# Optimization experiments

Hardware: AMD Instinct MI355X
Metric: run time of the kernel (lower is better)

## Reference

```python
import jax, jax.numpy as jnp
import numpy as np

B, T, D, H = 64, 257, 1024, 16
F = 4096
R = 16
HD = D // H


def _layer_norm(x, g, b, eps=1e-5):
    mu = x.mean(-1, keepdims=True)
    var = x.var(-1, keepdims=True)
    return (x - mu) / jnp.sqrt(var + eps) * g + b


def _quick_gelu(x):
    return x * jax.nn.sigmoid(1.702 * x)


def _attention(x, Wq, bq, Wk, bk, Wv, bv, Wo, bo):
    scale = HD ** -0.5
    q = (x @ Wq + bq) * scale
    k = x @ Wk + bk
    v = x @ Wv + bv
    q = q.reshape(B, T, H, HD).transpose(0, 2, 1, 3)
    k = k.reshape(B, T, H, HD).transpose(0, 2, 1, 3)
    v = v.reshape(B, T, H, HD).transpose(0, 2, 1, 3)
    attn = jax.nn.softmax(jnp.einsum('bhqd,bhkd->bhqk', q, k), axis=-1)
    o = jnp.einsum('bhqk,bhkd->bhqd', attn, v)
    o = o.transpose(0, 2, 1, 3).reshape(B, T, D)
    return o @ Wo + bo


def _match_indices(metric, r, class_token=True):
    # cosine-normalized bipartite matching (no-grad path in torch; index-only here)
    m = metric / jnp.linalg.norm(metric, axis=-1, keepdims=True)
    a, b = m[:, ::2, :], m[:, 1::2, :]        # [B, ta, D], [B, tb, D]
    scores = jnp.einsum('nac,nbc->nab', a, b)  # [B, ta, tb]
    if class_token:
        scores = scores.at[:, 0, :].set(-jnp.inf)
    node_max = scores.max(-1)
    node_idx = scores.argmax(-1)
    edge_idx = jnp.argsort(-node_max, axis=-1)  # descending
    unm_idx = edge_idx[:, r:]
    src_idx = edge_idx[:, :r]
    dst_idx = jnp.take_along_axis(node_idx, src_idx, axis=-1)
    if class_token:
        unm_idx = jnp.sort(unm_idx, axis=1)
    return unm_idx, src_idx, dst_idx


def _merge_sum(x, unm_idx, src_idx, dst_idx):
    src, dst = x[:, ::2, :], x[:, 1::2, :]
    c = x.shape[-1]
    unm = jnp.take_along_axis(src, unm_idx[..., None], axis=1)       # [B, ta-r, c]
    sel = jnp.take_along_axis(src, src_idx[..., None], axis=1)       # [B, r, c]
    dst = jax.vmap(lambda d, di, sv: d.at[di].add(sv))(dst, dst_idx, sel)
    return jnp.concatenate([unm, dst], axis=1)                       # [B, T-r, c]


def setup_inputs() -> dict:
    key = jax.random.key(0)
    ks = jax.random.split(key, 12)
    s = 0.02
    return {
        'hidden_states': jax.random.normal(ks[0], (B, T, D), jnp.float32),
        'ln1_g': jnp.ones((D,), jnp.float32),
        'ln1_b': jnp.zeros((D,), jnp.float32),
        'Wq': jax.random.normal(ks[1], (D, D), jnp.float32) * s,
        'bq': jnp.zeros((D,), jnp.float32),
        'Wk': jax.random.normal(ks[2], (D, D), jnp.float32) * s,
        'bk': jnp.zeros((D,), jnp.float32),
        'Wv': jax.random.normal(ks[3], (D, D), jnp.float32) * s,
        'bv': jnp.zeros((D,), jnp.float32),
        'Wo': jax.random.normal(ks[4], (D, D), jnp.float32) * s,
        'bo': jnp.zeros((D,), jnp.float32),
        'ln2_g': jnp.ones((D,), jnp.float32),
        'ln2_b': jnp.zeros((D,), jnp.float32),
        'W1': jax.random.normal(ks[5], (D, F), jnp.float32) * s,
        'b1': jnp.zeros((F,), jnp.float32),
        'W2': jax.random.normal(ks[6], (F, D), jnp.float32) * s,
        'b2': jnp.zeros((D,), jnp.float32),
    }


def reference(hidden_states, ln1_g, ln1_b, Wq, bq, Wk, bk, Wv, bv, Wo, bo,
              ln2_g, ln2_b, W1, b1, W2, b2):
    # 1) LN1 + self-attention + residual
    x = hidden_states + _attention(_layer_norm(hidden_states, ln1_g, ln1_b),
                                   Wq, bq, Wk, bk, Wv, bv, Wo, bo)
    # 2) ToMe merge with weighted average (initial size = ones -> merge_wavg)
    metric = jax.lax.stop_gradient(x)
    unm_idx, src_idx, dst_idx = _match_indices(metric, R, class_token=True)
    size = jnp.ones((B, T, 1), x.dtype)
    x = _merge_sum(x * size, unm_idx, src_idx, dst_idx)
    size = _merge_sum(size, unm_idx, src_idx, dst_idx)
    x = x / size
    # 3) LN2 + MLP (quick_gelu) + residual
    h = _layer_norm(x, ln2_g, ln2_b)
    h = _quick_gelu(h @ W1 + b1) @ W2 + b2
    return x + h  # [B, T - R, D]
```

## Files before the change

kernel.cpp:

```cpp
#include <hip/hip_runtime.h>
#include <math.h>

#define BB 64
#define TT 257
#define DD 1024
#define HH 16
#define FF 4096
#define RR 16
#define HDD 64
#define TMM 241
#define M1 (BB*TT)
#define M2 (BB*TMM)
#define NA 129
#define NB 128

typedef float f4v __attribute__((ext_vector_type(4)));
typedef short s8v __attribute__((ext_vector_type(8)));
typedef short s4v __attribute__((ext_vector_type(4)));
typedef unsigned short us;

__device__ __forceinline__ us f2bf(float f){
  unsigned u = __float_as_uint(f);
  u += 0x7fffu + ((u >> 16) & 1u);
  return (us)(u >> 16);
}
__device__ __forceinline__ float bf2f(us h){
  return __uint_as_float(((unsigned)h) << 16);
}
__device__ __forceinline__ void splitpk(float f0, float f1, unsigned &hp, unsigned &lp){
  unsigned u0 = __float_as_uint(f0), u1 = __float_as_uint(f1);
  unsigned h0m = u0 & 0xFFFF0000u, h1m = u1 & 0xFFFF0000u;
  hp = (u0 >> 16) | h1m;
  float l0 = f0 - __uint_as_float(h0m);
  float l1 = f1 - __uint_as_float(h1m);
  lp = (__float_as_uint(l0) >> 16) | (__float_as_uint(l1) & 0xFFFF0000u);
}
__device__ __forceinline__ void gl16(const us* g, us* l){
  __builtin_amdgcn_global_load_lds((const __attribute__((address_space(1))) void*)g,
                                   (__attribute__((address_space(3))) void*)l, 16, 0, 0);
}

__global__ __launch_bounds__(64) void lnstats_kernel(const float* __restrict__ x,
                                                     float* __restrict__ st)
{
  int row = blockIdx.x, lane = threadIdx.x;
  const float* p = x + (size_t)row * DD;
  float s = 0.0f, sq = 0.0f;
  #pragma unroll
  for (int i = 0; i < 4; i++){
    float4 v = *(const float4*)(p + i * 256 + lane * 4);
    s  += v.x + v.y + v.z + v.w;
    sq += v.x*v.x + v.y*v.y + v.z*v.z + v.w*v.w;
  }
  #pragma unroll
  for (int m = 1; m < 64; m <<= 1){ s += __shfl_xor(s, m); sq += __shfl_xor(sq, m); }
  if (lane == 0){
    float mu  = s * (1.0f / DD);
    float var = sq * (1.0f / DD) - mu * mu;
    st[2*row]     = mu;
    st[2*row + 1] = 1.0f / sqrtf(var + 1e-5f);
  }
}

__global__ __launch_bounds__(256) void lncvt_kernel(const float* __restrict__ x,
    const float* __restrict__ st, const float* __restrict__ g,
    const float* __restrict__ b, us* __restrict__ out)
{
  int row = blockIdx.x, tid = threadIdx.x;
  float mu = st[2*row], rstd = st[2*row + 1];
  float4 xv = *(const float4*)(x + (size_t)row * DD + tid * 4);
  float4 gv = *(const float4*)(g + tid * 4);
  float4 bv = *(const float4*)(b + tid * 4);
  s4v o;
  o[0] = (short)f2bf((xv.x - mu) * rstd * gv.x + bv.x);
  o[1] = (short)f2bf((xv.y - mu) * rstd * gv.y + bv.y);
  o[2] = (short)f2bf((xv.z - mu) * rstd * gv.z + bv.z);
  o[3] = (short)f2bf((xv.w - mu) * rstd * gv.w + bv.w);
  *(s4v*)(out + (size_t)row * DD + tid * 4) = o;
}

__global__ __launch_bounds__(256) void wt_kernel(const float* __restrict__ src,
                                                 us* __restrict__ dhi,
                                                 us* __restrict__ dlo,
                                                 const float* __restrict__ gscale,
                                                 int K, int N)
{
  __shared__ float t[32][33];
  int tx = threadIdx.x, ty = threadIdx.y;
  int n0 = blockIdx.x * 32, k0 = blockIdx.y * 32;
  #pragma unroll
  for (int r = 0; r < 4; r++)
    t[ty + 8*r][tx] = src[(size_t)(k0 + ty + 8*r) * N + n0 + tx];
  __syncthreads();
  float gs = gscale ? gscale[k0 + tx] : 1.0f;
  #pragma unroll
  for (int r = 0; r < 4; r++){
    float f = t[tx][ty + 8*r] * gs;
    us hi = f2bf(f);
    size_t o = (size_t)(n0 + ty + 8*r) * K + k0 + tx;
    dhi[o] = hi;
    if (dlo) dlo[o] = f2bf(f - bf2f(hi));
  }
}

__global__ __launch_bounds__(256) void qc_kernel(const float* __restrict__ Wq,
    const float* __restrict__ Wk, const float* __restrict__ Wv,
    const float* __restrict__ g, const float* __restrict__ b,
    float* __restrict__ c1, float* __restrict__ c2)
{
  __shared__ float p1[4][64], p2[4][64];
  int n0 = blockIdx.x * 64;
  int kind = n0 >> 10, col0 = n0 & 1023;
  const float* W = (kind == 0) ? Wq : (kind == 1) ? Wk : Wv;
  int tx = threadIdx.x & 63, ty = threadIdx.x >> 6;
  float s1 = 0.0f, s2 = 0.0f;
  for (int k = ty; k < 1024; k += 4){
    float w = W[(size_t)k * 1024 + col0 + tx];
    s1 += g[k] * w;
    s2 += b[k] * w;
  }
  p1[ty][tx] = s1; p2[ty][tx] = s2;
  __syncthreads();
  if (ty == 0){
    c1[n0 + tx] = p1[0][tx] + p1[1][tx] + p1[2][tx] + p1[3][tx];
    c2[n0 + tx] = p2[0][tx] + p2[1][tx] + p2[2][tx] + p2[3][tx];
  }
}

__global__ __launch_bounds__(512) void qkv_kernel(const float* __restrict__ hidden,
    const us* __restrict__ WBh, const us* __restrict__ WBl,
    const float* __restrict__ bq, const float* __restrict__ bk, const float* __restrict__ bv,
    const float* __restrict__ lnstat, const float* __restrict__ c1, const float* __restrict__ c2,
    us* __restrict__ qhp, us* __restrict__ qlp, us* __restrict__ khp,
    us* __restrict__ klp, us* __restrict__ vhp, us* __restrict__ vlp)
{
  const int M = M1, K = DD;
  __shared__ __align__(16) us Ah[128*40];
  __shared__ __align__(16) us Al[128*40];
  __shared__ __align__(16) us Bh[256*32];
  __shared__ __align__(16) us Bl[256*32];
  int tid = threadIdx.x;
  int m0 = blockIdx.y * 128, n0 = blockIdx.x * 256;
  int lane = tid & 63, w = tid >> 6;
  int wr = w >> 2, wc = w & 3;
  int fr = lane & 15, fq = lane >> 4;
  f4v acc[4][4];
  f4v zero = {0.0f, 0.0f, 0.0f, 0.0f};
  #pragma unroll
  for (int i = 0; i < 4; i++)
    #pragma unroll
    for (int j = 0; j < 4; j++) acc[i][j] = zero;
  int sr = tid >> 2, sc4 = (tid & 3) * 8;
  int ar = m0 + sr; if (ar >= M) ar = M - 1;
  int lr = lane >> 2, lc = (lane & 3) * 8;
  int gb0 = n0 + w*32 + lr;
  int swl = ((lr >> 1) & 3) << 3;
  int swr = ((fr >> 1) & 3) << 3;

  for (int kk = 0; kk < K; kk += 32){
    {
      const float* ap = hidden + (size_t)ar * K + kk + sc4;
      float4 fa = *(const float4*)(ap);
      float4 fb = *(const float4*)(ap + 4);
      unsigned h0, h1, h2, h3, l0, l1, l2, l3;
      splitpk(fa.x, fa.y, h0, l0);
      splitpk(fa.z, fa.w, h1, l1);
      splitpk(fb.x, fb.y, h2, l2);
      splitpk(fb.z, fb.w, h3, l3);
      uint4 hv = {h0, h1, h2, h3};
      uint4 lv = {l0, l1, l2, l3};
      *(uint4*)&Ah[sr*40 + sc4] = hv;
      *(uint4*)&Al[sr*40 + sc4] = lv;
    }
    gl16(WBh + (size_t)gb0 * K + kk + (lc ^ swl),        &Bh[(w*32)*32]);
    gl16(WBh + (size_t)(gb0 + 16) * K + kk + (lc ^ swl), &Bh[(w*32 + 16)*32]);
    gl16(WBl + (size_t)gb0 * K + kk + (lc ^ swl),        &Bl[(w*32)*32]);
    gl16(WBl + (size_t)(gb0 + 16) * K + kk + (lc ^ swl), &Bl[(w*32 + 16)*32]);
    __syncthreads();
    s8v ah[4], bh[4], al[4], bl[4];
    #pragma unroll
    for (int m = 0; m < 4; m++){
      ah[m] = *(const s8v*)&Ah[(wr*64 + m*16 + fr)*40 + fq*8];
      al[m] = *(const s8v*)&Al[(wr*64 + m*16 + fr)*40 + fq*8];
    }
    #pragma unroll
    for (int n = 0; n < 4; n++){
      bh[n] = *(const s8v*)&Bh[(wc*64 + n*16 + fr)*32 + (fq*8 ^ swr)];
      bl[n] = *(const s8v*)&Bl[(wc*64 + n*16 + fr)*32 + (fq*8 ^ swr)];
    }
    #pragma unroll
    for (int m = 0; m < 4; m++)
      #pragma unroll
      for (int n = 0; n < 4; n++){
        acc[m][n] = __builtin_amdgcn_mfma_f32_16x16x32_bf16(ah[m], bh[n], acc[m][n], 0, 0, 0);
        acc[m][n] = __builtin_amdgcn_mfma_f32_16x16x32_bf16(ah[m], bl[n], acc[m][n], 0, 0, 0);
        acc[m][n] = __builtin_amdgcn_mfma_f32_16x16x32_bf16(al[m], bh[n], acc[m][n], 0, 0, 0);
      }
    __syncthreads();
  }
  int kind = n0 >> 10;
  const float* bsel = (kind == 0) ? bq : (kind == 1) ? bk : bv;
  us* O0 = (kind == 0) ? qhp : (kind == 1) ? khp : vhp;
  us* O1 = (kind == 0) ? qlp : (kind == 1) ? klp : vlp;
  float scl = (kind == 0) ? 0.125f : 1.0f;
  float C1r[4], C2r[4];
  int h2r[4], d2r[4];
  #pragma unroll
  for (int n = 0; n < 4; n++){
    int gcol = n0 + wc*64 + n*16 + fr;
    int lcn = gcol & 1023;
    h2r[n] = lcn >> 6; d2r[n] = lcn & 63;
    C1r[n] = c1[gcol];
    C2r[n] = c2[gcol] + bsel[lcn];
  }
  #pragma unroll
  for (int m = 0; m < 4; m++){
    int grow0 = m0 + wr*64 + m*16 + fq*4;
    #pragma unroll
    for (int i = 0; i < 4; i++){
      int grow = grow0 + i;
      if (grow < M){
        float mu = lnstat[2*grow], rstd = lnstat[2*grow + 1];
        int b2 = grow / 257, t2 = grow - b2 * 257;
        size_t rb = ((size_t)(b2*16) * 257 + t2) * 64;
        #pragma unroll
        for (int n = 0; n < 4; n++){
          size_t off2 = rb + (size_t)h2r[n] * (257*64) + d2r[n];
          float v = (rstd * acc[m][n][i] - rstd * mu * C1r[n] + C2r[n]) * scl;
          us hi = f2bf(v);
          O0[off2] = hi;
          O1[off2] = f2bf(v - bf2f(hi));
        }
      }
    }
  }
}

template<int AMODE, int SPLIT, int EPI>
__global__ __launch_bounds__(256) void gemm2_kernel(const us* __restrict__ Ahp,
    const us* __restrict__ Alp,
    const us* __restrict__ BTh, const us* __restrict__ BTl,
    const float* __restrict__ bias, const float* __restrict__ resid,
    void* __restrict__ C0, int M, int N, int K)
{
  __shared__ __align__(16) us Ah[128*32];
  __shared__ __align__(16) us Bh[128*32];
  __shared__ __align__(16) us Al[SPLIT ? 128*32 : 8];
  __shared__ __align__(16) us Bl[SPLIT ? 128*32 : 8];
  int tid = threadIdx.x;
  int m0 = blockIdx.y * 128, n0 = blockIdx.x * 128;
  int lane = tid & 63, w = tid >> 6;
  int wr = w >> 1, wc = w & 1;
  int fr = lane & 15, fq = lane >> 4;
  f4v acc[4][4];
  f4v zero = {0.0f, 0.0f, 0.0f, 0.0f};
  #pragma unroll
  for (int i = 0; i < 4; i++)
    #pragma unroll
    for (int j = 0; j < 4; j++) acc[i][j] = zero;
  int lr = lane >> 2, lc = (lane & 3) * 8;
  int swl = ((lr >> 1) & 3) << 3;
  int swr = ((fr >> 1) & 3) << 3;
  int ga0 = m0 + w*32 + lr;      if (ga0 >= M) ga0 = M - 1;
  int ga1 = m0 + w*32 + 16 + lr; if (ga1 >= M) ga1 = M - 1;
  int gb0 = n0 + w*32 + lr;
  int b2a = ga0 / 257, t2a = ga0 - b2a * 257;
  int b2b = ga1 / 257, t2b = ga1 - b2b * 257;

  for (int kk = 0; kk < K; kk += 32){
    if (AMODE == 1){
      gl16(Ahp + (size_t)ga0 * K + kk + (lc ^ swl), &Ah[(w*32)*32]);
      gl16(Ahp + (size_t)ga1 * K + kk + (lc ^ swl), &Ah[(w*32 + 16)*32]);
      if (SPLIT){
        gl16(Alp + (size_t)ga0 * K + kk + (lc ^ swl), &Al[(w*32)*32]);
        gl16(Alp + (size_t)ga1 * K + kk + (lc ^ swl), &Al[(w*32 + 16)*32]);
      }
    } else {
      int h2 = kk >> 6, d2 = (kk & 63) + (lc ^ swl);
      size_t o0 = ((size_t)(b2a*16 + h2) * 257 + t2a) * 64 + d2;
      size_t o1 = ((size_t)(b2b*16 + h2) * 257 + t2b) * 64 + d2;
      gl16(Ahp + o0, &Ah[(w*32)*32]);
      gl16(Ahp + o1, &Ah[(w*32 + 16)*32]);
      if (SPLIT){
        gl16(Alp + o0, &Al[(w*32)*32]);
        gl16(Alp + o1, &Al[(w*32 + 16)*32]);
      }
    }
    gl16(BTh + (size_t)gb0 * K + kk + (lc ^ swl),        &Bh[(w*32)*32]);
    gl16(BTh + (size_t)(gb0 + 16) * K + kk + (lc ^ swl), &Bh[(w*32 + 16)*32]);
    if (SPLIT){
      gl16(BTl + (size_t)gb0 * K + kk + (lc ^ swl),        &Bl[(w*32)*32]);
      gl16(BTl + (size_t)(gb0 + 16) * K + kk + (lc ^ swl), &Bl[(w*32 + 16)*32]);
    }
    __syncthreads();
    s8v ah[4], bh[4], al[4], bl[4];
    #pragma unroll
    for (int m = 0; m < 4; m++){
      ah[m] = *(const s8v*)&Ah[(wr*64 + m*16 + fr)*32 + (fq*8 ^ swr)];
      if (SPLIT) al[m] = *(const s8v*)&Al[(wr*64 + m*16 + fr)*32 + (fq*8 ^ swr)];
    }
    #pragma unroll
    for (int n = 0; n < 4; n++){
      bh[n] = *(const s8v*)&Bh[(wc*64 + n*16 + fr)*32 + (fq*8 ^ swr)];
      if (SPLIT) bl[n] = *(const s8v*)&Bl[(wc*64 + n*16 + fr)*32 + (fq*8 ^ swr)];
    }
    #pragma unroll
    for (int m = 0; m < 4; m++)
      #pragma unroll
      for (int n = 0; n < 4; n++){
        acc[m][n] = __builtin_amdgcn_mfma_f32_16x16x32_bf16(ah[m], bh[n], acc[m][n], 0, 0, 0);
        if (SPLIT){
          acc[m][n] = __builtin_amdgcn_mfma_f32_16x16x32_bf16(ah[m], bl[n], acc[m][n], 0, 0, 0);
          acc[m][n] = __builtin_amdgcn_mfma_f32_16x16x32_bf16(al[m], bh[n], acc[m][n], 0, 0, 0);
        }
      }
    __syncthreads();
  }
  #pragma unroll
  for (int m = 0; m < 4; m++){
    int grow0 = m0 + wr*64 + m*16 + fq*4;
    #pragma unroll
    for (int n = 0; n < 4; n++){
      int gcol = n0 + wc*64 + n*16 + fr;
      float bcol = bias[gcol];
      #pragma unroll
      for (int i = 0; i < 4; i++){
        int grow = grow0 + i;
        if (grow < M){
          float v = acc[m][n][i] + bcol;
          size_t off = (size_t)grow * N + gcol;
          if (EPI == 1){
            ((float*)C0)[off] = v + resid[off];
          } else {
            float gq = v / (1.0f + expf(-1.702f * v));
            ((us*)C0)[off] = f2bf(gq);
          }
        }
      }
    }
  }
}

template<int EPI>
__global__ __launch_bounds__(512) void gemm8p_kernel(const us* __restrict__ A,
    const us* __restrict__ B, const float* __restrict__ bias,
    const float* __restrict__ resid, void* __restrict__ C, int M, int N, int K)
{
  __shared__ __align__(16) us As[3][256*32];
  __shared__ __align__(16) us Bs[3][256*32];
  int tid = threadIdx.x;
  int m0 = blockIdx.y * 256, n0 = blockIdx.x * 256;
  int lane = tid & 63, w = tid >> 6;
  int wr = w >> 2, wc = w & 3;
  int fr = lane & 15, fq = lane >> 4;
  f4v acc[8][4];
  f4v zero = {0.0f, 0.0f, 0.0f, 0.0f};
  #pragma unroll
  for (int i = 0; i < 8; i++)
    #pragma unroll
    for (int j = 0; j < 4; j++) acc[i][j] = zero;
  int srow = w*16 + (lane >> 2);
  int aR0 = m0 + srow;        if (aR0 >= M) aR0 = M - 1;
  int aR1 = m0 + 128 + srow;  if (aR1 >= M) aR1 = M - 1;
  int bR0 = n0 + srow;
  int bR1 = n0 + 128 + srow;
  int o16 = ((lane & 3) * 8) ^ (((srow >> 1) & 3) << 3);
  int swr = ((fr >> 1) & 3) << 3;
  int ldst = w * 512;

  const int NT = K >> 5;
  #pragma unroll
  for (int t0 = 0; t0 < 2; t0++){
    gl16(A + (size_t)aR0 * K + t0*32 + o16, &As[t0][ldst]);
    gl16(B + (size_t)bR0 * K + t0*32 + o16, &Bs[t0][ldst]);
    gl16(A + (size_t)aR1 * K + t0*32 + o16, &As[t0][4096 + ldst]);
    gl16(B + (size_t)bR1 * K + t0*32 + o16, &Bs[t0][4096 + ldst]);
  }
  asm volatile("s_waitcnt vmcnt(4)" ::: "memory");
  __builtin_amdgcn_s_barrier();

  int buf = 0;
  #pragma unroll 1
  for (int t = 0; t < NT; ++t){
    int nbuf = buf + 2; if (nbuf >= 3) nbuf -= 3;
    bool pf = (t + 2) < NT;
    int kk2 = (t + 2) * 32;
    us* Ab = As[buf];
    us* Bb = Bs[buf];
    {
      s8v a[4], b[4];
      #pragma unroll
      for (int mt = 0; mt < 4; mt++){
        int r = wr*128 + mt*16 + fr;
        a[mt] = *(const s8v*)&Ab[r*32 + (fq*8 ^ swr)];
      }
      #pragma unroll
      for (int nt = 0; nt < 4; nt++){
        int r = wc*64 + nt*16 + fr;
        b[nt] = *(const s8v*)&Bb[r*32 + (fq*8 ^ swr)];
      }
      if (pf){
        gl16(A + (size_t)aR0 * K + kk2 + o16, &As[nbuf][ldst]);
        gl16(B + (size_t)bR0 * K + kk2 + o16, &Bs[nbuf][ldst]);
      }
      __builtin_amdgcn_s_barrier();
      __builtin_amdgcn_s_setprio(1);
      #pragma unroll
      for (int mt = 0; mt < 4; mt++)
        #pragma unroll
        for (int nt = 0; nt < 4; nt++)
          acc[mt][nt] = __builtin_amdgcn_mfma_f32_16x16x32_bf16(a[mt], b[nt], acc[mt][nt], 0, 0, 0);
      __builtin_amdgcn_s_setprio(0);
      __builtin_amdgcn_s_barrier();
    }
    {
      s8v a[4], b[4];
      #pragma unroll
      for (int mt = 0; mt < 4; mt++){
        int r = wr*128 + 64 + mt*16 + fr;
        a[mt] = *(const s8v*)&Ab[r*32 + (fq*8 ^ swr)];
      }
      #pragma unroll
      for (int nt = 0; nt < 4; nt++){
        int r = wc*64 + nt*16 + fr;
        b[nt] = *(const s8v*)&Bb[r*32 + (fq*8 ^ swr)];
      }
      if (pf){
        gl16(A + (size_t)aR1 * K + kk2 + o16, &As[nbuf][4096 + ldst]);
        gl16(B + (size_t)bR1 * K + kk2 + o16, &Bs[nbuf][4096 + ldst]);
      }
      __builtin_amdgcn_s_barrier();
      __builtin_amdgcn_s_setprio(1);
      #pragma unroll
      for (int mt = 0; mt < 4; mt++)
        #pragma unroll
        for (int nt = 0; nt < 4; nt++)
          acc[4 + mt][nt] = __builtin_amdgcn_mfma_f32_16x16x32_bf16(a[mt], b[nt], acc[4 + mt][nt], 0, 0, 0);
      __builtin_amdgcn_s_setprio(0);
    }
    if (t + 1 < NT){
      if (pf) asm volatile("s_waitcnt vmcnt(4)" ::: "memory");
      else    asm volatile("s_waitcnt vmcnt(0)" ::: "memory");
    }
    __builtin_amdgcn_s_barrier();
    buf = buf + 1; if (buf >= 3) buf = 0;
  }
  #pragma unroll
  for (int mh = 0; mh < 2; mh++)
    #pragma unroll
    for (int mt = 0; mt < 4; mt++){
      int grow0 = m0 + wr*128 + mh*64 + mt*16 + fq*4;
      #pragma unroll
      for (int nt = 0; nt < 4; nt++){
        int gcol = n0 + wc*64 + nt*16 + fr;
        float bcol = bias[gcol];
        #pragma unroll
        for (int i = 0; i < 4; i++){
          int grow = grow0 + i;
          if (grow < M){
            float v = acc[mh*4 + mt][nt][i] + bcol;
            size_t off = (size_t)grow * N + gcol;
            if (EPI == 1){
              ((float*)C)[off] = v + resid[off];
            } else {
              float gq = v / (1.0f + expf(-1.702f * v));
              ((us*)C)[off] = f2bf(gq);
            }
          }
        }
      }
    }
}

__global__ __launch_bounds__(512, 1) void attn_flash_kernel(
    const us* __restrict__ Qh, const us* __restrict__ Ql,
    const us* __restrict__ Kh, const us* __restrict__ Klo,
    const us* __restrict__ Vh, const us* __restrict__ Vlo,
    us* Oh, us* Ol)
{
  __shared__ __align__(16) us Kl[257 * 128];
  __shared__ __align__(16) us Vl[64 * 640];
  int bh = blockIdx.x;
  const size_t hb = (size_t)bh * 257 * 64;
  int tid = threadIdx.x;
  int l = tid & 63, w = tid >> 6;
  int g = l >> 4, c = l & 15;
  const float NEG = -3.0e38f;

  {
    s8v z8 = {0,0,0,0,0,0,0,0};
    for (int idx = tid; idx < 64*640/8; idx += 512)
      *((s8v*)Vl + idx) = z8;
  }
  __syncthreads();
  for (int idx = tid; idx < 257*8; idx += 512){
    int tok = idx >> 3, ch = idx & 7;
    int sw = (tok & 7) << 4;
    s8v hv = *(const s8v*)(Kh  + hb + (size_t)tok * 64 + ch*8);
    s8v lv = *(const s8v*)(Klo + hb + (size_t)tok * 64 + ch*8);
    char* kr = (char*)Kl + tok * 256;
    *(s8v*)(kr + ((ch*16) ^ sw)) = hv;
    *(s8v*)(kr + 128 + ((ch*16) ^ sw)) = lv;
  }
  for (int idx = tid; idx < 257*8; idx += 512){
    int tok = idx >> 3, ch = idx & 7;
    s8v hv = *(const s8v*)(Vh  + hb + (size_t)tok * 64 + ch*8);
    s8v lv = *(const s8v*)(Vlo + hb + (size_t)tok * 64 + ch*8);
    #pragma unroll
    for (int j = 0; j < 8; j++){
      int d = ch*8 + j;
      char* vr = (char*)Vl + d * 1280;
      int off = (tok * 2) ^ (j << 4);
      *(us*)(vr + off) = (us)hv[j];
      *(us*)(vr + 640 + off) = (us)lv[j];
    }
  }
  __syncthreads();

  for (int qt = w; qt < 17; qt += 8){
    int t0 = qt * 16;
    int qr = t0 + c; if (qr > 256) qr = 256;
    const us* qp  = Qh + hb + (size_t)qr * 64 + g*8;
    const us* qp2 = Ql + hb + (size_t)qr * 64 + g*8;
    s8v qhi[2], qlo[2];
    qhi[0] = *(const s8v*)(qp);       qhi[1] = *(const s8v*)(qp + 32);
    qlo[0] = *(const s8v*)(qp2);      qlo[1] = *(const s8v*)(qp2 + 32);

    float m_run = NEG, l_run = 0.0f;
    f4v o4[4];
    #pragma unroll
    for (int dt = 0; dt < 4; dt++) o4[dt] = (f4v){0.0f, 0.0f, 0.0f, 0.0f};

    #pragma unroll 1
    for (int mck = 0; mck < 9; mck++){
      f4v a0, a1;
      {
        int t = 2*mck;
        int krow = t * 16 + c; if (krow > 256) krow = 256;
        char* kr = (char*)Kl + krow * 256;
        int sw = (krow & 7) << 4;
        s8v khi0 = *(const s8v*)(kr + ((g * 16) ^ sw));
        s8v khi1 = *(const s8v*)(kr + ((64 + g * 16) ^ sw));
        s8v klo0 = *(const s8v*)(kr + 128 + ((g * 16) ^ sw));
        s8v klo1 = *(const s8v*)(kr + 128 + ((64 + g * 16) ^ sw));
        f4v a = {0.0f, 0.0f, 0.0f, 0.0f};
        a = __builtin_amdgcn_mfma_f32_16x16x32_bf16(khi0, qhi[0], a, 0, 0, 0);
        a = __builtin_amdgcn_mfma_f32_16x16x32_bf16(khi1, qhi[1], a, 0, 0, 0);
        a = __builtin_amdgcn_mfma_f32_16x16x32_bf16(khi0, qlo[0], a, 0, 0, 0);
        a = __builtin_amdgcn_mfma_f32_16x16x32_bf16(khi1, qlo[1], a, 0, 0, 0);
        a = __builtin_amdgcn_mfma_f32_16x16x32_bf16(klo0, qhi[0], a, 0, 0, 0);
        a = __builtin_amdgcn_mfma_f32_16x16x32_bf16(klo1, qhi[1], a, 0, 0, 0);
        a0 = a;
      }
      if (mck < 8){
        int t = 2*mck + 1;
        int krow = t * 16 + c; if (krow > 256) krow = 256;
        char* kr = (char*)Kl + krow * 256;
        int sw = (krow & 7) << 4;
        s8v khi0 = *(const s8v*)(kr + ((g * 16) ^ sw));
        s8v khi1 = *(const s8v*)(kr + ((64 + g * 16) ^ sw));
        s8v klo0 = *(const s8v*)(kr + 128 + ((g * 16) ^ sw));
        s8v klo1 = *(const s8v*)(kr + 128 + ((64 + g * 16) ^ sw));
        f4v a = {0.0f, 0.0f, 0.0f, 0.0f};
        a = __builtin_amdgcn_mfma_f32_16x16x32_bf16(khi0, qhi[0], a, 0, 0, 0);
        a = __builtin_amdgcn_mfma_f32_16x16x32_bf16(khi1, qhi[1], a, 0, 0, 0);
        a = __builtin_amdgcn_mfma_f32_16x16x32_bf16(khi0, qlo[0], a, 0, 0, 0);
        a = __builtin_amdgcn_mfma_f32_16x16x32_bf16(khi1, qlo[1], a, 0, 0, 0);
        a = __builtin_amdgcn_mfma_f32_16x16x32_bf16(klo0, qhi[0], a, 0, 0, 0);
        a = __builtin_amdgcn_mfma_f32_16x16x32_bf16(klo1, qhi[1], a, 0, 0, 0);
        a1 = a;
      } else {
        a1 = (f4v){NEG, NEG, NEG, NEG};
        a0[0] = (g == 0) ? a0[0] : NEG;
        a0[1] = NEG; a0[2] = NEG; a0[3] = NEG;
      }
      float cm = fmaxf(fmaxf(fmaxf(a0[0], a0[1]), fmaxf(a0[2], a0[3])),
                       fmaxf(fmaxf(a1[0], a1[1]), fmaxf(a1[2], a1[3])));
      cm = fmaxf(cm, __shfl_xor(cm, 16));
      cm = fmaxf(cm, __shfl_xor(cm, 32));
      float m_new = fmaxf(m_run, cm);
      float scl = __expf(m_run - m_new);
      m_run = m_new;
      l_run *= scl;
      #pragma unroll
      for (int dt = 0; dt < 4; dt++){
        o4[dt][0] *= scl; o4[dt][1] *= scl; o4[dt][2] *= scl; o4[dt][3] *= scl;
      }
      float ls = 0.0f;
      unsigned Ph2[2][2], Pl2[2][2];
      #pragma unroll
      for (int k2 = 0; k2 < 2; k2++){
        float e0 = __expf(a0[2*k2] - m_new), e1 = __expf(a0[2*k2+1] - m_new);
        ls += e0 + e1;
        us h0 = f2bf(e0), h1 = f2bf(e1);
        Ph2[0][k2] = (unsigned)h0 | ((unsigned)h1 << 16);
        Pl2[0][k2] = (unsigned)f2bf(e0 - bf2f(h0)) | ((unsigned)f2bf(e1 - bf2f(h1)) << 16);
        float e2 = __expf(a1[2*k2] - m_new), e3 = __expf(a1[2*k2+1] - m_new);
        ls += e2 + e3;
        us h2 = f2bf(e2), h3 = f2bf(e3);
        Ph2[1][k2] = (unsigned)h2 | ((unsigned)h3 << 16);
        Pl2[1][k2] = (unsigned)f2bf(e2 - bf2f(h2)) | ((unsigned)f2bf(e3 - bf2f(h3)) << 16);
      }
      l_run += ls;
      s8v pbh, pbl;
      #pragma unroll
      for (int ww = 0; ww < 4; ww++){
        int srcl = (((g & 1) * 2 + (ww >> 1)) << 4) | c;
        unsigned h0 = (unsigned)__shfl((int)Ph2[0][ww & 1], srcl, 64);
        unsigned lo0 = (unsigned)__shfl((int)Pl2[0][ww & 1], srcl, 64);
        unsigned h1 = (unsigned)__shfl((int)Ph2[1][ww & 1], srcl, 64);
        unsigned lo1 = (unsigned)__shfl((int)Pl2[1][ww & 1], srcl, 64);
        ((unsigned*)&pbh)[ww] = (g >> 1) ? h1 : h0;
        ((unsigned*)&pbl)[ww] = (g >> 1) ? lo1 : lo0;
      }
      #pragma unroll
      for (int dt = 0; dt < 4; dt++){
        int d = dt * 16 + c;
        char* vr = (char*)Vl + d * 1280;
        int off = (mck * 64 + g * 16) ^ ((d & 7) << 4);
        s8v vh = *(const s8v*)(vr + off);
        s8v vlo = *(const s8v*)(vr + 640 + off);
        o4[dt] = __builtin_amdgcn_mfma_f32_16x16x32_bf16(vh, pbh, o4[dt], 0, 0, 0);
        o4[dt] = __builtin_amdgcn_mfma_f32_16x16x32_bf16(vh, pbl, o4[dt], 0, 0, 0);
        o4[dt] = __builtin_amdgcn_mfma_f32_16x16x32_bf16(vlo, pbh, o4[dt], 0, 0, 0);
      }
    }
    l_run += __shfl_xor(l_run, 16);
    l_run += __shfl_xor(l_run, 32);
    float inv = 1.0f / l_run;
    int qrow = t0 + c;
    if (qrow <= 256){
      us* oph = Oh + hb + (size_t)qrow * 64;
      us* opl = Ol + hb + (size_t)qrow * 64;
      #pragma unroll
      for (int dt = 0; dt < 4; dt++){
        s4v hv4, lv4;
        #pragma unroll
        for (int i = 0; i < 4; i++){
          float ov = o4[dt][i] * inv;
          us hi = f2bf(ov);
          hv4[i] = (short)hi;
          lv4[i] = (short)f2bf(ov - bf2f(hi));
        }
        *(s4v*)(oph + dt*16 + g*4) = hv4;
        *(s4v*)(opl + dt*16 + g*4) = lv4;
      }
    }
  }
}

__global__ __launch_bounds__(64) void norms_kernel(const float* __restrict__ x, float* __restrict__ nrm)
{
  int row = blockIdx.x, lane = threadIdx.x;
  const float* p = x + (size_t)row * DD;
  float sq = 0.0f;
  #pragma unroll
  for (int i = 0; i < 4; i++){
    float4 v = *(const float4*)(p + i * 256 + lane * 4);
    sq += v.x*v.x + v.y*v.y + v.z*v.z + v.w*v.w;
  }
  #pragma unroll
  for (int m = 1; m < 64; m <<= 1) sq += __shfl_xor(sq, m);
  if (lane == 0) nrm[row] = sqrtf(sq);
}

__global__ __launch_bounds__(256) void scores_kernel(const float* __restrict__ x,
                                                     const float* __restrict__ nrm,
                                                     float* __restrict__ sc)
{
  __shared__ __align__(16) float as_[16][1028];
  __shared__ __align__(16) float bs_[16][1028];
  int it = blockIdx.x, b = blockIdx.y;
  int tid = threadIdx.x;
  int rloc = tid >> 4, chunk = tid & 15;
  {
    int i = it * 16 + rloc;
    int tg = (i < NA) ? 2 * i : 2 * (NA - 1);
    const float* p = x + ((size_t)b * TT + tg) * DD + chunk * 64;
    #pragma unroll
    for (int ii = 0; ii < 16; ii++)
      *(float4*)&as_[rloc][chunk * 64 + 4*ii] = *(const float4*)(p + 4*ii);
  }
  for (int jt = 0; jt < 8; jt++){
    __syncthreads();
    {
      int j = jt * 16 + rloc;
      const float* p = x + ((size_t)b * TT + 2*j + 1) * DD + chunk * 64;
      #pragma unroll
      for (int ii = 0; ii < 16; ii++)
        *(float4*)&bs_[rloc][chunk * 64 + 4*ii] = *(const float4*)(p + 4*ii);
    }
    __syncthreads();
    int iloc = tid >> 4, jloc = tid & 15;
    float sum = 0.0f;
    #pragma unroll 8
    for (int cgg = 0; cgg < 1024; cgg += 4){
      float4 av = *(const float4*)&as_[iloc][cgg];
      float4 bvv = *(const float4*)&bs_[jloc][cgg];
      sum += av.x*bvv.x + av.y*bvv.y + av.z*bvv.z + av.w*bvv.w;
    }
    int i = it * 16 + iloc, j = jt * 16 + jloc;
    if (i < NA){
      float val = sum / (nrm[(size_t)b * TT + 2*i] * nrm[(size_t)b * TT + 2*j + 1]);
      sc[((size_t)b * NA + i) * NB + j] = val;
    }
  }
}

__global__ __launch_bounds__(64) void node_kernel(const float* __restrict__ sc,
                                                  float* __restrict__ nmax, int* __restrict__ nidx)
{
  int i = blockIdx.x, b = blockIdx.y, lane = threadIdx.x;
  const float* row = sc + ((size_t)b * NA + i) * NB;
  float v0 = row[lane];
  float v1 = row[lane + 64];
  float bv = v0; int bi = lane;
  if (v1 > bv){ bv = v1; bi = lane + 64; }
  #pragma unroll
  for (int m = 1; m < 64; m <<= 1){
    float ov = __shfl_xor(bv, m);
    int oi = __shfl_xor(bi, m);
    if (ov > bv || (ov == bv && oi < bi)){ bv = ov; bi = oi; }
  }
  if (lane == 0){
    if (i == 0){ nmax[(size_t)b * NA] = -INFINITY; nidx[(size_t)b * NA] = 0; }
    else { nmax[(size_t)b * NA + i] = bv; nidx[(size_t)b * NA + i] = bi; }
  }
}

__global__ __launch_bounds__(256) void rank_kernel(const float* __restrict__ nmax,
    const int* __restrict__ nidx, int* __restrict__ src, int* __restrict__ dst,
    int* __restrict__ unm, int* __restrict__ cnt)
{
  __shared__ float v[NA];
  __shared__ int rk[NA];
  __shared__ int edge[NA];
  __shared__ int cs[NB];
  int b = blockIdx.x, t = threadIdx.x;
  if (t < NA) v[t] = nmax[(size_t)b * NA + t];
  if (t < NB) cs[t] = 0;
  __syncthreads();
  if (t < NA){
    float vt = v[t]; int r = 0;
    for (int i = 0; i < NA; i++){
      float vi = v[i];
      r += (vi > vt) || (vi == vt && i < t);
    }
    rk[t] = r; edge[r] = t;
  }
  __syncthreads();
  if (t < RR){
    int s = edge[t];
    src[b * RR + t] = s;
    int d = nidx[(size_t)b * NA + s];
    dst[b * RR + t] = d;
    atomicAdd(&cs[d], 1);
  }
  if (t < NA && rk[t] >= RR){
    int p = 0;
    for (int i = 0; i < NA; i++) p += (i < t) && (rk[i] >= RR);
    unm[b * (NA - RR) + p] = t;
  }
  __syncthreads();
  if (t < NB) cnt[b * NB + t] = cs[t];
}

__global__ __launch_bounds__(256) void merge_kernel(const float* __restrict__ x,
    const int* __restrict__ src, const int* __restrict__ dst, const int* __restrict__ unm,
    const int* __restrict__ cnt, float* __restrict__ xm)
{
  int u = blockIdx.x, b = blockIdx.y;
  int c = threadIdx.x * 4;
  const float* xb = x + (size_t)b * TT * DD;
  float4 acc;
  if (u < NA - RR){
    int ts = 2 * unm[b * (NA - RR) + u];
    acc = *(const float4*)(xb + (size_t)ts * DD + c);
  } else {
    int j = u - (NA - RR);
    acc = *(const float4*)(xb + (size_t)(2*j + 1) * DD + c);
    #pragma unroll
    for (int k2 = 0; k2 < RR; k2++){
      if (dst[b * RR + k2] == j){
        int ts = 2 * src[b * RR + k2];
        float4 av = *(const float4*)(xb + (size_t)ts * DD + c);
        acc.x += av.x; acc.y += av.y; acc.z += av.z; acc.w += av.w;
      }
    }
    float inv = 1.0f / (float)(1 + cnt[b * NB + j]);
    acc.x *= inv; acc.y *= inv; acc.z *= inv; acc.w *= inv;
  }
  *(float4*)(xm + ((size_t)b * TMM + u) * DD + c) = acc;
}

extern "C" void kernel_launch(void* const* d_in, const int* in_sizes, int n_in,
                              void* d_out, int out_size, void* d_ws, size_t ws_size,
                              hipStream_t stream)
{
  (void)in_sizes; (void)n_in; (void)out_size; (void)ws_size;
  const float* hidden = (const float*)d_in[0];
  const float* ln1_g  = (const float*)d_in[1];
  const float* ln1_b  = (const float*)d_in[2];
  const float* Wq = (const float*)d_in[3];
  const float* bq = (const float*)d_in[4];
  const float* Wk = (const float*)d_in[5];
  const float* bk = (const float*)d_in[6];
  const float* Wv = (const float*)d_in[7];
  const float* bv = (const float*)d_in[8];
  const float* Wo = (const float*)d_in[9];
  const float* bo = (const float*)d_in[10];
  const float* ln2_g = (const float*)d_in[11];
  const float* ln2_b = (const float*)d_in[12];
  const float* W1 = (const float*)d_in[13];
  const float* b1 = (const float*)d_in[14];
  const float* W2 = (const float*)d_in[15];
  const float* b2 = (const float*)d_in[16];

  char* base = (char*)d_ws;
  const size_t PE = (size_t)M1 * DD;
  const size_t PL = PE * sizeof(us);
  us* qh = (us*)base;          us* ql = qh + PE;
  us* kh = (us*)(base + 2*PL); us* kl = kh + PE;
  us* vh = (us*)(base + 4*PL); us* vl = vh + PE;
  us* wts = (us*)(base + 6*PL);
  const size_t WD = (size_t)DD * DD;
  us* wqh = wts;
  us* wkh = wqh + WD;
  us* wvh = wkh + WD;
  us* wql = wvh + WD;
  us* wkl = wql + WD;
  us* wvl = wkl + WD;
  us* woh = wvl + WD;
  us* wol = woh + WD;
  us* w1h = wol + WD;
  us* w2h = w1h + (size_t)DD * FF;
  float* lnst1 = (float*)(w2h + (size_t)FF * DD);
  float* c1p   = lnst1 + 2 * M1;
  float* c2p   = c1p + 3072;
  float* xb = (float*)(base + 2*PL);
  float* nrm   = (float*)(base + 4*PL);
  float* sc    = nrm + M1;
  float* nmaxp = sc + (size_t)BB * NA * NB;
  int*   nidxp = (int*)(nmaxp + BB * NA);
  int*   srcI  = nidxp + BB * NA;
  int*   dstI  = srcI + BB * RR;
  int*   unmI  = dstI + BB * RR;
  int*   cntI  = unmI + BB * (NA - RR);
  us*    xh2   = (us*)(base + 4*PL + (size_t)8*1024*1024);
  float* lnst2 = (float*)(base + 4*PL + (size_t)48*1024*1024);
  float* xm = (float*)d_out;
  us* mid = (us*)base;

  dim3 tb32(32, 8);
  wt_kernel<<<dim3(DD/32, DD/32), tb32, 0, stream>>>(Wq, wqh, wql, ln1_g, DD, DD);
  wt_kernel<<<dim3(DD/32, DD/32), tb32, 0, stream>>>(Wk, wkh, wkl, ln1_g, DD, DD);
  wt_kernel<<<dim3(DD/32, DD/32), tb32, 0, stream>>>(Wv, wvh, wvl, ln1_g, DD, DD);
  wt_kernel<<<dim3(DD/32, DD/32), tb32, 0, stream>>>(Wo, woh, wol, nullptr, DD, DD);
  wt_kernel<<<dim3(FF/32, DD/32), tb32, 0, stream>>>(W1, w1h, nullptr, nullptr, DD, FF);
  wt_kernel<<<dim3(DD/32, FF/32), tb32, 0, stream>>>(W2, w2h, nullptr, nullptr, FF, DD);

  qc_kernel<<<48, 256, 0, stream>>>(Wq, Wk, Wv, ln1_g, ln1_b, c1p, c2p);
  lnstats_kernel<<<M1, 64, 0, stream>>>(hidden, lnst1);

  qkv_kernel<<<dim3(3072/256, (M1 + 127)/128), 512, 0, stream>>>(hidden, wqh, wql,
      bq, bk, bv, lnst1, c1p, c2p, qh, ql, kh, kl, vh, vl);

  attn_flash_kernel<<<BB*HH, 512, 0, stream>>>(qh, ql, kh, kl, vh, vl, qh, ql);

  gemm2_kernel<2,1,1><<<dim3(DD/128, (M1 + 127)/128), 256, 0, stream>>>(qh, ql, woh, wol,
      bo, hidden, xb, M1, DD, DD);

  norms_kernel<<<M1, 64, 0, stream>>>(xb, nrm);
  scores_kernel<<<dim3(9, BB), 256, 0, stream>>>(xb, nrm, sc);
  node_kernel<<<dim3(NA, BB), 64, 0, stream>>>(sc, nmaxp, nidxp);
  rank_kernel<<<BB, 256, 0, stream>>>(nmaxp, nidxp, srcI, dstI, unmI, cntI);
  merge_kernel<<<dim3(TMM, BB), 256, 0, stream>>>(xb, srcI, dstI, unmI, cntI, xm);

  lnstats_kernel<<<M2, 64, 0, stream>>>(xm, lnst2);
  lncvt_kernel<<<M2, 256, 0, stream>>>(xm, lnst2, ln2_g, ln2_b, xh2);

  gemm8p_kernel<2><<<dim3(FF/256, (M2 + 255)/256), 512, 0, stream>>>(xh2, w1h,
      b1, nullptr, mid, M2, FF, DD);
  gemm8p_kernel<1><<<dim3(DD/256, (M2 + 255)/256), 512, 0, stream>>>(mid, w2h,
      b2, xm, (float*)d_out, M2, DD, FF);
}
```

Before: 1.559 ms.

## Compute ToMe similarity scores with split-bf16 MFMA instead of fp32 FMA

The output projection epilogue now stores the residual-added activations as a hi/lo bf16 pair instead of fp32. The cosine-similarity scores are then computed by a new MFMA kernel that uses three bf16 products (hh, hl, lh) to approximate fp32 accuracy, replacing the scalar fp32 dot-product kernel. The norms and merge kernels read the split pair and reconstruct fp32. The change moves the scores work onto matrix cores and halves per-tensor byte width, at the cost of two extra MFMAs per tile, a small loss of precision in the reconstructed activations, and only 128 blocks for the scores launch.

After: 1.392 ms, median of 2. 1.12x faster.

```diff
diff --git a/kernel.cpp b/kernel.cpp
--- a/kernel.cpp
+++ b/kernel.cpp
@@ -34,6 +34,12 @@
   float l0 = f0 - __uint_as_float(h0m);
   float l1 = f1 - __uint_as_float(h1m);
   lp = (__float_as_uint(l0) >> 16) | (__float_as_uint(l1) & 0xFFFF0000u);
+}
+__device__ __forceinline__ void split1(float f, us &h, us &l){
+  unsigned u = __float_as_uint(f);
+  unsigned hm = u & 0xFFFF0000u;
+  h = (us)(u >> 16);
+  l = (us)(__float_as_uint(f - __uint_as_float(hm)) >> 16);
 }
 __device__ __forceinline__ void gl16(const us* g, us* l){
   __builtin_amdgcn_global_load_lds((const __attribute__((address_space(1))) void*)g,
@@ -241,7 +247,7 @@
     const us* __restrict__ Alp,
     const us* __restrict__ BTh, const us* __restrict__ BTl,
     const float* __restrict__ bias, const float* __restrict__ resid,
-    void* __restrict__ C0, int M, int N, int K)
+    void* __restrict__ C0, void* __restrict__ C1, int M, int N, int K)
 {
   __shared__ __align__(16) us Ah[128*32];
   __shared__ __align__(16) us Bh[128*32];
@@ -331,9 +337,15 @@
           size_t off = (size_t)grow * N + gcol;
           if (EPI == 1){
             ((float*)C0)[off] = v + resid[off];
-          } else {
+          } else if (EPI == 2){
             float gq = v / (1.0f + expf(-1.702f * v));
             ((us*)C0)[off] = f2bf(gq);
+          } else {
+            float x = v + resid[off];
+            us h, l;
+            split1(x, h, l);
+            ((us*)C0)[off] = h;
+            ((us*)C1)[off] = l;
           }
         }
       }
@@ -649,60 +661,103 @@
   }
 }
 
-__global__ __launch_bounds__(64) void norms_kernel(const float* __restrict__ x, float* __restrict__ nrm)
+__global__ __launch_bounds__(64) void norms_kernel(const us* __restrict__ xh,
+    const us* __restrict__ xl, float* __restrict__ nrm)
 {
   int row = blockIdx.x, lane = threadIdx.x;
-  const float* p = x + (size_t)row * DD;
+  const us* ph = xh + (size_t)row * DD + lane * 16;
+  const us* pl = xl + (size_t)row * DD + lane * 16;
   float sq = 0.0f;
   #pragma unroll
-  for (int i = 0; i < 4; i++){
-    float4 v = *(const float4*)(p + i * 256 + lane * 4);
-    sq += v.x*v.x + v.y*v.y + v.z*v.z + v.w*v.w;
+  for (int i = 0; i < 2; i++){
+    s8v h = *(const s8v*)(ph + i * 8);
+    s8v l = *(const s8v*)(pl + i * 8);
+    #pragma unroll
+    for (int j = 0; j < 8; j++){
+      float v = bf2f((us)h[j]) + bf2f((us)l[j]);
+      sq += v * v;
+    }
   }
   #pragma unroll
   for (int m = 1; m < 64; m <<= 1) sq += __shfl_xor(sq, m);
   if (lane == 0) nrm[row] = sqrtf(sq);
 }
 
-__global__ __launch_bounds__(256) void scores_kernel(const float* __restrict__ x,
-                                                     const float* __restrict__ nrm,
-                                                     float* __restrict__ sc)
-{
-  __shared__ __align__(16) float as_[16][1028];
-  __shared__ __align__(16) float bs_[16][1028];
-  int it = blockIdx.x, b = blockIdx.y;
+__global__ __launch_bounds__(256) void scores8_kernel(const us* __restrict__ xh,
+    const us* __restrict__ xl, const float* __restrict__ nrm, float* __restrict__ sc)
+{
+  __shared__ __align__(16) us Ah[128*32];
+  __shared__ __align__(16) us Al[128*32];
+  __shared__ __align__(16) us Bh[128*32];
+  __shared__ __align__(16) us Bl[128*32];
+  int mblk = blockIdx.x, b = blockIdx.y;
+  const size_t rb = (size_t)b * TT * DD;
   int tid = threadIdx.x;
-  int rloc = tid >> 4, chunk = tid & 15;
-  {
-    int i = it * 16 + rloc;
-    int tg = (i < NA) ? 2 * i : 2 * (NA - 1);
-    const float* p = x + ((size_t)b * TT + tg) * DD + chunk * 64;
-    #pragma unroll
-    for (int ii = 0; ii < 16; ii++)
-      *(float4*)&as_[rloc][chunk * 64 + 4*ii] = *(const float4*)(p + 4*ii);
-  }
-  for (int jt = 0; jt < 8; jt++){
+  int lane = tid & 63, w = tid >> 6;
+  int wr = w >> 1, wc = w & 1;
+  int fr = lane & 15, fq = lane >> 4;
+  f4v acc[4][4];
+  f4v zero = {0.0f, 0.0f, 0.0f, 0.0f};
+  #pragma unroll
+  for (int i = 0; i < 4; i++)
+    #pragma unroll
+    for (int j = 0; j < 4; j++) acc[i][j] = zero;
+  int lr = lane >> 2, lc = (lane & 3) * 8;
+  int swl = ((lr >> 1) & 3) << 3;
+  int swr = ((fr >> 1) & 3) << 3;
+  int ra0 = mblk*128 + w*32 + lr;      if (ra0 > 128) ra0 = 128;
+  int ra1 = mblk*128 + w*32 + 16 + lr; if (ra1 > 128) ra1 = 128;
+  size_t ta0 = (size_t)(2 * ra0) * DD, ta1 = (size_t)(2 * ra1) * DD;
+  size_t tb0 = (size_t)(2 * (w*32 + lr) + 1) * DD;
+  size_t tb1 = (size_t)(2 * (w*32 + 16 + lr) + 1) * DD;
+
+  for (int kk = 0; kk < DD; kk += 32){
+    int co = kk + (lc ^ swl);
+    gl16(xh + rb + ta0 + co, &Ah[(w*32)*32]);
+    gl16(xh + rb + ta1 + co, &Ah[(w*32 + 16)*32]);
+    gl16(xl + rb + ta0 + co, &Al[(w*32)*32]);
+    gl16(xl + rb + ta1 + co, &Al[(w*32 + 16)*32]);
+    gl16(xh + rb + tb0 + co, &Bh[(w*32)*32]);
+    gl16(xh + rb + tb1 + co, &Bh[(w*32 + 16)*32]);
+    gl16(xl + rb + tb0 + co, &Bl[(w*32)*32]);
+    gl16(xl + rb + tb1 + co, &Bl[(w*32 + 16)*32]);
     __syncthreads();
-    {
-      int j = jt * 16 + rloc;
-      const float* p = x + ((size_t)b * TT + 2*j + 1) * DD + chunk * 64;
-      #pragma unroll
-      for (int ii = 0; ii < 16; ii++)
-        *(float4*)&bs_[rloc][chunk * 64 + 4*ii] = *(const float4*)(p + 4*ii);
-    }
+    s8v ah[4], bh[4], al[4], bl[4];
+    #pragma unroll
+    for (int m = 0; m < 4; m++){
+      ah[m] = *(const s8v*)&Ah[(wr*64 + m*16 + fr)*32 + (fq*8 ^ swr)];
+      al[m] = *(const s8v*)&Al[(wr*64 + m*16 + fr)*32 + (fq*8 ^ swr)];
+    }
+    #pragma unroll
+    for (int n = 0; n < 4; n++){
+      bh[n] = *(const s8v*)&Bh[(wc*64 + n*16 + fr)*32 + (fq*8 ^ swr)];
+      bl[n] = *(const s8v*)&Bl[(wc*64 + n*16 + fr)*32 + (fq*8 ^ swr)];
+    }
+    #pragma unroll
+    for (int m = 0; m < 4; m++)
+      #pragma unroll
+      for (int n = 0; n < 4; n++){
+        acc[m][n] = __builtin_amdgcn_mfma_f32_16x16x32_bf16(ah[m], bh[n], acc[m][n], 0, 0, 0);
+        acc[m][n] = __builtin_amdgcn_mfma_f32_16x16x32_bf16(ah[m], bl[n], acc[m][n], 0, 0, 0);
+        acc[m][n] = __builtin_amdgcn_mfma_f32_16x16x32_bf16(al[m], bh[n], acc[m][n], 0, 0, 0);
+      }
     __syncthreads();
-    int iloc = tid >> 4, jloc = tid & 15;
-    float sum = 0.0f;
-    #pragma unroll 8
-    for (int cgg = 0; cgg < 1024; cgg += 4){
-      float4 av = *(const float4*)&as_[iloc][cgg];
-      float4 bvv = *(const float4*)&bs_[jloc][cgg];
-      sum += av.x*bvv.x + av.y*bvv.y + av.z*bvv.z + av.w*bvv.w;
-    }
-    int i = it * 16 + iloc, j = jt * 16 + jloc;
-    if (i < NA){
-      float val = sum / (nrm[(size_t)b * TT + 2*i] * nrm[(size_t)b * TT + 2*j + 1]);
-      sc[((size_t)b * NA + i) * NB + j] = val;
+  }
+  #pragma unroll
+  for (int m = 0; m < 4; m++){
+    int grow0 = mblk*128 + wr*64 + m*16 + fq*4;
+    #pragma unroll
+    for (int n = 0; n < 4; n++){
+      int gcol = wc*64 + n*16 + fr;
+      float no = nrm[(size_t)b * TT + 2*gcol + 1];
+      #pragma unroll
+      for (int i = 0; i < 4; i++){
+        int grow = grow0 + i;
+        if (grow < NA){
+          float ne = nrm[(size_t)b * TT + 2*grow];
+          sc[((size_t)b * NA + grow) * NB + gcol] = acc[m][n][i] / (ne * no);
+        }
+      }
     }
   }
 }
@@ -765,26 +820,42 @@
   if (t < NB) cnt[b * NB + t] = cs[t];
 }
 
-__global__ __launch_bounds__(256) void merge_kernel(const float* __restrict__ x,
+__global__ __launch_bounds__(256) void merge_kernel(const us* __restrict__ xh,
+    const us* __restrict__ xl,
     const int* __restrict__ src, const int* __restrict__ dst, const int* __restrict__ unm,
     const int* __restrict__ cnt, float* __restrict__ xm)
 {
   int u = blockIdx.x, b = blockIdx.y;
   int c = threadIdx.x * 4;
-  const float* xb = x + (size_t)b * TT * DD;
+  const us* xhb = xh + (size_t)b * TT * DD;
+  const us* xlb = xl + (size_t)b * TT * DD;
   float4 acc;
   if (u < NA - RR){
     int ts = 2 * unm[b * (NA - RR) + u];
-    acc = *(const float4*)(xb + (size_t)ts * DD + c);
+    s4v h = *(const s4v*)(xhb + (size_t)ts * DD + c);
+    s4v l = *(const s4v*)(xlb + (size_t)ts * DD + c);
+    acc.x = bf2f((us)h[0]) + bf2f((us)l[0]);
+    acc.y = bf2f((us)h[1]) + bf2f((us)l[1]);
+    acc.z = bf2f((us)h[2]) + bf2f((us)l[2]);
+    acc.w = bf2f((us)h[3]) + bf2f((us)l[3]);
   } else {
     int j = u - (NA - RR);
-    acc = *(const float4*)(xb + (size_t)(2*j + 1) * DD + c);
+    s4v h = *(const s4v*)(xhb + (size_t)(2*j + 1) * DD + c);
+    s4v l = *(const s4v*)(xlb + (size_t)(2*j + 1) * DD + c);
+    acc.x = bf2f((us)h[0]) + bf2f((us)l[0]);
+    acc.y = bf2f((us)h[1]) + bf2f((us)l[1]);
+    acc.z = bf2f((us)h[2]) + bf2f((us)l[2]);
+    acc.w = bf2f((us)h[3]) + bf2f((us)l[3]);
     #pragma unroll
     for (int k2 = 0; k2 < RR; k2++){
       if (dst[b * RR + k2] == j){
         int ts = 2 * src[b * RR + k2];
-        float4 av = *(const float4*)(xb + (size_t)ts * DD + c);
-        acc.x += av.x; acc.y += av.y; acc.z += av.z; acc.w += av.w;
+        s4v ah4 = *(const s4v*)(xhb + (size_t)ts * DD + c);
+        s4v al4 = *(const s4v*)(xlb + (size_t)ts * DD + c);
+        acc.x += bf2f((us)ah4[0]) + bf2f((us)al4[0]);
+        acc.y += bf2f((us)ah4[1]) + bf2f((us)al4[1]);
+        acc.z += bf2f((us)ah4[2]) + bf2f((us)al4[2]);
+        acc.w += bf2f((us)ah4[3]) + bf2f((us)al4[3]);
       }
     }
     float inv = 1.0f / (float)(1 + cnt[b * NB + j]);
@@ -837,7 +908,8 @@
   float* lnst1 = (float*)(w2h + (size_t)FF * DD);
   float* c1p   = lnst1 + 2 * M1;
   float* c2p   = c1p + 3072;
-  float* xb = (float*)(base + 2*PL);
+  us* xbh = (us*)(base + 2*PL);
+  us* xbl = xbh + PE;
   float* nrm   = (float*)(base + 4*PL);
   float* sc    = nrm + M1;
   float* nmaxp = sc + (size_t)BB * NA * NB;
@@ -867,14 +939,14 @@
 
   attn_flash_kernel<<<BB*HH, 512, 0, stream>>>(qh, ql, kh, kl, vh, vl, qh, ql);
 
-  gemm2_kernel<2,1,1><<<dim3(DD/128, (M1 + 127)/128), 256, 0, stream>>>(qh, ql, woh, wol,
-      bo, hidden, xb, M1, DD, DD);
-
-  norms_kernel<<<M1, 64, 0, stream>>>(xb, nrm);
-  scores_kernel<<<dim3(9, BB), 256, 0, stream>>>(xb, nrm, sc);
+  gemm2_kernel<2,1,3><<<dim3(DD/128, (M1 + 127)/128), 256, 0, stream>>>(qh, ql, woh, wol,
+      bo, hidden, xbh, xbl, M1, DD, DD);
+
+  norms_kernel<<<M1, 64, 0, stream>>>(xbh, xbl, nrm);
+  scores8_kernel<<<dim3(2, BB), 256, 0, stream>>>(xbh, xbl, nrm, sc);
   node_kernel<<<dim3(NA, BB), 64, 0, stream>>>(sc, nmaxp, nidxp);
   rank_kernel<<<BB, 256, 0, stream>>>(nmaxp, nidxp, srcI, dstI, unmI, cntI);
-  merge_kernel<<<dim3(TMM, BB), 256, 0, stream>>>(xb, srcI, dstI, unmI, cntI, xm);
+  merge_kernel<<<dim3(TMM, BB), 256, 0, stream>>>(xbh, xbl, srcI, dstI, unmI, cntI, xm);
 
   lnstats_kernel<<<M2, 64, 0, stream>>>(xm, lnst2);
   lncvt_kernel<<<M2, 256, 0, stream>>>(xm, lnst2, ln2_g, ln2_b, xh2);
```
